# Performance work log

Hardware: AMD Instinct MI355X
Metric: run time of the kernel (lower is better)

The kernel has to match this reference:

```python
import jax, jax.numpy as jnp
import numpy as np
from math import sqrt

N_HEAD = 16
W_SCALE = 0.02  # keep pre-softmax logits in a sane range

def setup_inputs() -> dict:
    key = jax.random.key(0)
    ks = jax.random.split(key, 7)
    B, T, C = 2, 2048, 1024
    QL, KVL = 512, 512
    return {
        "x":     jax.random.normal(ks[0], (B, T, C), dtype=jnp.float32),
        "W_dq":  jax.random.normal(ks[1], (QL, C),  dtype=jnp.float32) * W_SCALE,
        "W_uq":  jax.random.normal(ks[2], (C, QL),  dtype=jnp.float32) * W_SCALE,
        "W_dkv": jax.random.normal(ks[3], (KVL, C), dtype=jnp.float32) * W_SCALE,
        "W_uk":  jax.random.normal(ks[4], (C, KVL), dtype=jnp.float32) * W_SCALE,
        "W_uv":  jax.random.normal(ks[5], (C, KVL), dtype=jnp.float32) * W_SCALE,
        "W_o":   jax.random.normal(ks[6], (C, C),   dtype=jnp.float32) * W_SCALE,
    }

def reference(x, W_dq, W_uq, W_dkv, W_uk, W_uv, W_o):
    B, T, C = x.shape
    nh = N_HEAD
    hs = C // nh
    n_kvl = W_dkv.shape[0]

    # absorbed matrices (training path of the torch module)
    # k_eff: (W_dq^T @ W_uq^T @ W_uk) -> (C, n_kvl) -> (nh, hs, n_kvl)
    k_eff = (W_dq.T @ W_uq.T @ W_uk).reshape(nh, hs, n_kvl)
    # v_eff: (W_uv^T @ W_o^T) -> (n_kvl, C) -> (n_kvl, nh, hs) -> (nh, n_kvl, hs)
    v_eff = jnp.transpose((W_uv.T @ W_o.T).reshape(n_kvl, nh, hs), (1, 0, 2))

    c_kv = x @ W_dkv.T                      # (B, T, n_kvl) latent KV cache
    q = (x @ W_dq.T) @ W_uq.T               # (B, T, C)
    q = q.reshape(B, T, nh, hs)             # (B, T, nh, hs)

    # scores: q @ k_eff @ c_kv^T / sqrt(hs) -> (B, nh, T, T)
    q_lat = jnp.einsum('bqhd,hdl->bhql', q, k_eff)
    attn = jnp.einsum('bhql,bkl->bhqk', q_lat, c_kv) / sqrt(hs)

    causal = jnp.tril(jnp.ones((T, T), dtype=bool))
    attn = jnp.where(causal[None, None], attn, -jnp.inf)
    attn = jax.nn.softmax(attn, axis=-1)    # dropout p=0.0

    # y = attn @ c_kv @ v_eff (W_o is absorbed into v_eff)
    y_lat = jnp.einsum('bhqk,bkl->bhql', attn, c_kv)
    y = jnp.einsum('bhql,hld->bqhd', y_lat, v_eff).reshape(B, T, C)
    return (y, c_kv)
```

## Files before the change

kernel.cpp:

```cpp
#include <hip/hip_runtime.h>
#include <hip/hip_bf16.h>


using bf16 = __hip_bfloat16;
using u32  = unsigned int;
using short8 = __attribute__((ext_vector_type(8))) short;
using f4     = __attribute__((ext_vector_type(4))) float;

static constexpr int kB  = 2;
static constexpr int kT  = 2048;
static constexpr int kC  = 1024;
static constexpr int kNH = 16;
static constexpr int kL  = 512;

__device__ inline u32 f2bf2(float a, float b) {
  bf16 ha = __float2bfloat16(a), hb = __float2bfloat16(b);
  unsigned short ua, ub;
  __builtin_memcpy(&ua, &ha, 2);
  __builtin_memcpy(&ub, &hb, 2);
  return (u32)ua | ((u32)ub << 16);
}
__device__ inline unsigned short f2bf(float x) {
  bf16 h = __float2bfloat16(x);
  unsigned short u; __builtin_memcpy(&u, &h, 2);
  return u;
}
__device__ inline short8 frag_ld(const void* p) {
  short8 r; __builtin_memcpy(&r, p, 16); return r;
}
__device__ inline void g2lds16(const bf16* g, bf16* l) {
  __builtin_amdgcn_global_load_lds(
      (const __attribute__((address_space(1))) u32*)g,
      (__attribute__((address_space(3))) u32*)l, 16, 0, 0);
}

__global__ __launch_bounds__(256)
void casts_merged(const float* __restrict__ x,   const float* __restrict__ wdq,
                  const float* __restrict__ wuq, const float* __restrict__ wdkv,
                  const float* __restrict__ wo,  const float* __restrict__ wuk,
                  const float* __restrict__ wuv,
                  bf16* __restrict__ xb,   bf16* __restrict__ wdqb,
                  bf16* __restrict__ wuqb, bf16* __restrict__ wdkvb,
                  bf16* __restrict__ wob,
                  bf16* __restrict__ uqT, bf16* __restrict__ ukT,
                  bf16* __restrict__ uvT, bf16* __restrict__ dqT)
{
  __shared__ float s[32][33];
  const int id = blockIdx.x;
  if (id < 6656) {
    long i = (long)(id * 256 + threadIdx.x) * 4;
    const float* sp; bf16* d; long off;
    if      (i < 4194304) { sp = x;    d = xb;    off = i; }
    else if (i < 4718592) { sp = wdq;  d = wdqb;  off = i - 4194304; }
    else if (i < 5242880) { sp = wuq;  d = wuqb;  off = i - 4718592; }
    else if (i < 5767168) { sp = wdkv; d = wdkvb; off = i - 5242880; }
    else                  { sp = wo;   d = wob;   off = i - 5767168; }
    float4 v = *(const float4*)(sp + off);
    *(uint2*)((u32*)d + off / 2) = make_uint2(f2bf2(v.x, v.y), f2bf2(v.z, v.w));
  } else {
    const int t = id - 6656;
    const int z = t >> 10, xy = t & 1023;
    const float* src = z == 0 ? wuq : z == 1 ? wuk : z == 2 ? wuv : wdq;
    bf16* dst        = z == 0 ? uqT : z == 1 ? ukT : z == 2 ? uvT : dqT;
    const int R = (z == 3) ? 512 : 1024, C = (z == 3) ? 1024 : 512;
    const int r0 = (xy & 31) * 32, c0 = (xy >> 5) * 32;
    if (r0 >= R || c0 >= C) return;
    const int xl = threadIdx.x & 31, y = threadIdx.x >> 5;
#pragma unroll
    for (int i = 0; i < 4; ++i)
      s[y*4 + i][xl] = src[(long)(r0 + y*4 + i) * C + c0 + xl];
    __syncthreads();
    unsigned short* dp = (unsigned short*)dst;
#pragma unroll
    for (int i = 0; i < 4; ++i)
      dp[(long)(c0 + y*4 + i) * R + r0 + xl] = f2bf(s[xl][y*4 + i]);
  }
}

__global__ __launch_bounds__(256)
void upcast_kernel(const bf16* __restrict__ qc, float* __restrict__ dst)
{
  int i = (blockIdx.x * 256 + threadIdx.x) * 4;
  if (i < 2097152) {
    int row = i >> 9, col = i & 511;
    uint2 v = *(const uint2*)((const u32*)(qc + (long)row * 1024 + 512 + col));
    float4 o;
    o.x = __uint_as_float(v.x << 16);
    o.y = __uint_as_float(v.x & 0xffff0000u);
    o.z = __uint_as_float(v.y << 16);
    o.w = __uint_as_float(v.y & 0xffff0000u);
    *(float4*)(dst + i) = o;
  }
}

template<typename TCe>
__global__ __launch_bounds__(256)
void mm_nt(const bf16* __restrict__ A, int lda, long aHi, long aLo,
           const bf16* __restrict__ Bm, int ldb, long bHi, long bLo,
           TCe* __restrict__ Cm, int ldc, long cHi, long cLo,
           int K, float alpha)
{
  const int z = blockIdx.z;
  A  += (long)(z >> 4) * aHi + (long)(z & 15) * aLo;
  Bm += (long)(z >> 4) * bHi + (long)(z & 15) * bLo;
  Cm += (long)(z >> 4) * cHi + (long)(z & 15) * cLo;

  __shared__ __align__(16) bf16 As[64][72];
  __shared__ __align__(16) bf16 Bs[64][72];

  const int tid = threadIdx.x;
  const int w = tid >> 6, lane = tid & 63;
  const int quad = lane >> 4, lp = lane & 15;
  const int m0 = blockIdx.x * 64, n0 = blockIdx.y * 64;
  const int row = tid >> 2, cseg = (tid & 3) * 16;

  f4 acc[4];
#pragma unroll
  for (int i = 0; i < 4; ++i) acc[i] = f4{0.f, 0.f, 0.f, 0.f};

  for (int k0 = 0; k0 < K; k0 += 64) {
    const bf16* ag = A  + (long)(m0 + row) * lda + k0 + cseg;
    const bf16* bg = Bm + (long)(n0 + row) * ldb + k0 + cseg;
    uint4 a0 = *(const uint4*)ag, a1 = *(const uint4*)(ag + 8);
    uint4 b0 = *(const uint4*)bg, b1 = *(const uint4*)(bg + 8);
    __syncthreads();
    *(uint4*)&As[row][cseg] = a0; *(uint4*)&As[row][cseg + 8] = a1;
    *(uint4*)&Bs[row][cseg] = b0; *(uint4*)&Bs[row][cseg + 8] = b1;
    __syncthreads();

    short8 af0 = frag_ld(&As[w*16 + lp][quad * 8]);
    short8 af1 = frag_ld(&As[w*16 + lp][32 + quad * 8]);
#pragma unroll
    for (int nb = 0; nb < 4; ++nb) {
      short8 bf0 = frag_ld(&Bs[nb*16 + lp][quad * 8]);
      short8 bf1 = frag_ld(&Bs[nb*16 + lp][32 + quad * 8]);
      acc[nb] = __builtin_amdgcn_mfma_f32_16x16x32_bf16(af0, bf0, acc[nb], 0, 0, 0);
      acc[nb] = __builtin_amdgcn_mfma_f32_16x16x32_bf16(af1, bf1, acc[nb], 0, 0, 0);
    }
  }
#pragma unroll
  for (int nb = 0; nb < 4; ++nb)
#pragma unroll
    for (int r = 0; r < 4; ++r) {
      float v = alpha * acc[nb][r];
      long off = (long)(m0 + w*16 + quad*4 + r) * ldc + n0 + nb*16 + lp;
      if constexpr (__is_same(TCe, float)) Cm[off] = v;
      else ((unsigned short*)Cm)[off] = f2bf(v);
    }
}

__global__ __launch_bounds__(256)
void mega1(const bf16* __restrict__ xb,   const bf16* __restrict__ wdq,
           const bf16* __restrict__ wukT, const bf16* __restrict__ wuqT,
           const bf16* __restrict__ wo,   const bf16* __restrict__ wuvT,
           bf16* __restrict__ qc, bf16* __restrict__ tmpT,
           bf16* __restrict__ v_effT)
{
  const int id = blockIdx.x;
  const bf16 *A, *Bm; bf16* Cm;
  int lda, ldb, ldc, m0, n0;
  if (id < 1024) {
    m0 = (id & 63) * 64; n0 = (id >> 6) * 64;
    A = xb;   lda = 1024; Bm = wdq;  ldb = 1024; Cm = qc;     ldc = 1024;
  } else if (id < 1088) {
    const int t = id - 1024;
    m0 = (t & 7) * 64; n0 = (t >> 3) * 64;
    A = wukT; lda = 1024; Bm = wuqT; ldb = 1024; Cm = tmpT;   ldc = 512;
  } else {
    const int t = id - 1088;
    m0 = (t & 15) * 64; n0 = (t >> 4) * 64;
    A = wo;   lda = 1024; Bm = wuvT; ldb = 1024; Cm = v_effT; ldc = 512;
  }

  __shared__ __align__(16) bf16 As[64][72];
  __shared__ __align__(16) bf16 Bs[64][72];

  const int tid = threadIdx.x;
  const int w = tid >> 6, lane = tid & 63;
  const int quad = lane >> 4, lp = lane & 15;
  const int row = tid >> 2, cseg = (tid & 3) * 16;

  f4 acc[4];
#pragma unroll
  for (int i = 0; i < 4; ++i) acc[i] = f4{0.f, 0.f, 0.f, 0.f};

  for (int k0 = 0; k0 < 1024; k0 += 64) {
    const bf16* ag = A  + (long)(m0 + row) * lda + k0 + cseg;
    const bf16* bg = Bm + (long)(n0 + row) * ldb + k0 + cseg;
    uint4 a0 = *(const uint4*)ag, a1 = *(const uint4*)(ag + 8);
    uint4 b0 = *(const uint4*)bg, b1 = *(const uint4*)(bg + 8);
    __syncthreads();
    *(uint4*)&As[row][cseg] = a0; *(uint4*)&As[row][cseg + 8] = a1;
    *(uint4*)&Bs[row][cseg] = b0; *(uint4*)&Bs[row][cseg + 8] = b1;
    __syncthreads();

    short8 af0 = frag_ld(&As[w*16 + lp][quad * 8]);
    short8 af1 = frag_ld(&As[w*16 + lp][32 + quad * 8]);
#pragma unroll
    for (int nb = 0; nb < 4; ++nb) {
      short8 bf0 = frag_ld(&Bs[nb*16 + lp][quad * 8]);
      short8 bf1 = frag_ld(&Bs[nb*16 + lp][32 + quad * 8]);
      acc[nb] = __builtin_amdgcn_mfma_f32_16x16x32_bf16(af0, bf0, acc[nb], 0, 0, 0);
      acc[nb] = __builtin_amdgcn_mfma_f32_16x16x32_bf16(af1, bf1, acc[nb], 0, 0, 0);
    }
  }
#pragma unroll
  for (int nb = 0; nb < 4; ++nb)
#pragma unroll
    for (int r = 0; r < 4; ++r) {
      long off = (long)(m0 + w*16 + quad*4 + r) * ldc + n0 + nb*16 + lp;
      ((unsigned short*)Cm)[off] = f2bf(acc[nb][r]);
    }
}

__global__ __launch_bounds__(256)
void gemm_multi(const bf16* __restrict__ qc,   const bf16* __restrict__ wuq,
                const bf16* __restrict__ keff, const bf16* __restrict__ veff,
                bf16* __restrict__ qfull, bf16* __restrict__ Kh,
                bf16* __restrict__ Vh, float kScale)
{
  const int id = blockIdx.x;
  const bf16 *A, *Bm; bf16* Cm;
  int lda, ldb, ldc, m0, n0; float alpha;
  if (id < 256) {
    m0 = (id >> 3) * 128; n0 = (id & 7) * 128;
    A = qc;        lda = 1024; Bm = wuq;  ldb = 512;
    Cm = qfull;    ldc = 1024; alpha = 1.0f;
  } else if (id < 512) {
    const int t = id - 256;
    m0 = (t >> 3) * 128; n0 = (t & 7) * 128;
    A = qc + 512;  lda = 1024; Bm = keff; ldb = 512;
    Cm = Kh;       ldc = 1024; alpha = kScale;
  } else {
    const int t = id - 512;
    const int b = t >> 7, tt = t & 127;
    m0 = (tt >> 4) * 128; n0 = (tt & 15) * 128;
    A = veff;      lda = 512;
    Bm = qc + (long)b * kT * 1024 + 512; ldb = 1024;
    Cm = Vh + (long)b * 1024 * kT;       ldc = kT; alpha = 1.0f;
  }

  __shared__ __align__(16) bf16 As[128 * 64];
  __shared__ __align__(16) bf16 Bs[128 * 64];

  const int tid = threadIdx.x;
  const int w = tid >> 6, lane = tid & 63;
  const int quad = lane >> 4, lp = lane & 15;
  const int wm = w >> 1, wn = w & 1;

  const int srow = lane >> 3;
  const int scol = ((lane & 7) ^ srow) * 8;
  const bf16* aSrc = A  + (long)(m0 + w * 32 + srow) * lda + scol;
  const bf16* bSrc = Bm + (long)(n0 + w * 32 + srow) * ldb + scol;
  bf16* aDst = As + w * 32 * 64;
  bf16* bDst = Bs + w * 32 * 64;

  f4 acc[4][4];
#pragma unroll
  for (int mi = 0; mi < 4; ++mi)
#pragma unroll
    for (int ni = 0; ni < 4; ++ni) acc[mi][ni] = f4{0.f, 0.f, 0.f, 0.f};

  const int swz = lp & 7;
  const int aRow = (wm * 64 + lp) * 64;
  const int bRow = (wn * 64 + lp) * 64;
  const int c0 = (quad       ^ swz) * 8;
  const int c1 = ((quad + 4) ^ swz) * 8;

  for (int k0 = 0; k0 < 512; k0 += 64) {
#pragma unroll
    for (int i = 0; i < 4; ++i) {
      g2lds16(aSrc + k0 + (long)(i * 8) * lda, aDst + i * 8 * 64);
      g2lds16(bSrc + k0 + (long)(i * 8) * ldb, bDst + i * 8 * 64);
    }
    asm volatile("s_waitcnt vmcnt(0)" ::: "memory");
    __builtin_amdgcn_s_barrier();

    short8 af0[4], af1[4], bf0[4], bf1[4];
#pragma unroll
    for (int mi = 0; mi < 4; ++mi) {
      af0[mi] = frag_ld(&As[aRow + mi * 1024 + c0]);
      af1[mi] = frag_ld(&As[aRow + mi * 1024 + c1]);
    }
#pragma unroll
    for (int ni = 0; ni < 4; ++ni) {
      bf0[ni] = frag_ld(&Bs[bRow + ni * 1024 + c0]);
      bf1[ni] = frag_ld(&Bs[bRow + ni * 1024 + c1]);
    }
#pragma unroll
    for (int mi = 0; mi < 4; ++mi)
#pragma unroll
      for (int ni = 0; ni < 4; ++ni) {
        acc[mi][ni] = __builtin_amdgcn_mfma_f32_16x16x32_bf16(
            af0[mi], bf0[ni], acc[mi][ni], 0, 0, 0);
        acc[mi][ni] = __builtin_amdgcn_mfma_f32_16x16x32_bf16(
            af1[mi], bf1[ni], acc[mi][ni], 0, 0, 0);
      }
    __builtin_amdgcn_s_barrier();
  }

#pragma unroll
  for (int mi = 0; mi < 4; ++mi)
#pragma unroll
    for (int ni = 0; ni < 4; ++ni)
#pragma unroll
      for (int r = 0; r < 4; ++r) {
        float v = alpha * acc[mi][ni][r];
        long off = (long)(m0 + wm*64 + mi*16 + quad*4 + r) * ldc
                 + n0 + wn*64 + ni*16 + lp;
        ((unsigned short*)Cm)[off] = f2bf(v);
      }
}

__global__ __launch_bounds__(512, 6)
void flash64(const bf16* __restrict__ qfull, const bf16* __restrict__ Kh,
             const bf16* __restrict__ VhT, float* __restrict__ y)
{
  const int id = blockIdx.x;
  const int j = id & 255, hi2 = id >> 8;
  const int h = j >> 4, sl = j & 15;
  const int s = hi2 ? (15 - sl) : sl;
  const int b = hi2;
  const int tid = threadIdx.x;
  const int w = tid >> 6, lane = tid & 63;
  const int quad = lane >> 4, lp = lane & 15;

  __shared__ __align__(16) bf16 Kt[2][64 * 64];
  __shared__ __align__(16) bf16 Vt[2][64 * 64];
  __shared__ __align__(16) bf16 Pb[8][16 * 72];

  bf16* Pw = &Pb[w][0];

  const long bh = (long)b * kNH + h;
  const int q0 = s * 128 + w * 16;

  const bf16* qp = qfull + ((long)b * kT + q0 + lp) * kC + h * 64 + quad * 8;
  const short8 qf0 = frag_ld(qp);
  const short8 qf1 = frag_ld(qp + 32);

  const int rk = w * 8 + (lane >> 3), blk = lane & 7;
  const int soff = ((blk ^ (rk & 7)) * 8);
  const bf16* kSrc = Kh + ((long)b * kT + rk) * kC + h * 64 + soff;
  const bf16* vSrc = VhT + (bh * 64 + rk) * (long)kT + soff;

  const int swz = lp & 7;
  const int lp64 = lp * 64;
  const int B0 = ((0 + quad) ^ swz) * 8;
  const int B1 = ((4 + quad) ^ swz) * 8;

  const int tmaxw = 2 * s + ((w >> 2) ? 1 : 0);
  const int nt = 2 * s + 2;

  f4 O0 = f4{0,0,0,0}, O1 = f4{0,0,0,0}, O2 = f4{0,0,0,0}, O3 = f4{0,0,0,0};
  float m_r = -3e38f, l_r = 0.f;

  g2lds16(kSrc, &Kt[0][w * 512]);
  g2lds16(vSrc, &Vt[0][w * 512]);
  asm volatile("s_waitcnt vmcnt(0)" ::: "memory");
  __builtin_amdgcn_s_barrier();
  __builtin_amdgcn_sched_barrier(0);

  for (int t = 0; t < nt; ++t) {
    const int bf = t & 1;
    if (t + 1 < nt) {
      g2lds16(kSrc + (long)(t + 1) * 65536, &Kt[bf ^ 1][w * 512]);
      g2lds16(vSrc + (t + 1) * 64,          &Vt[bf ^ 1][w * 512]);
    }

    if (t <= tmaxw) {
      const bf16* KB = &Kt[bf][0];
      f4 s0 = f4{0,0,0,0}, s1 = f4{0,0,0,0}, s2 = f4{0,0,0,0}, s3 = f4{0,0,0,0};
      {
        short8 a;
        a = frag_ld(KB +    0 + lp64 + B0); s0 = __builtin_amdgcn_mfma_f32_16x16x32_bf16(a, qf0, s0, 0, 0, 0);
        a = frag_ld(KB +    0 + lp64 + B1); s0 = __builtin_amdgcn_mfma_f32_16x16x32_bf16(a, qf1, s0, 0, 0, 0);
        a = frag_ld(KB + 1024 + lp64 + B0); s1 = __builtin_amdgcn_mfma_f32_16x16x32_bf16(a, qf0, s1, 0, 0, 0);
        a = frag_ld(KB + 1024 + lp64 + B1); s1 = __builtin_amdgcn_mfma_f32_16x16x32_bf16(a, qf1, s1, 0, 0, 0);
        a = frag_ld(KB + 2048 + lp64 + B0); s2 = __builtin_amdgcn_mfma_f32_16x16x32_bf16(a, qf0, s2, 0, 0, 0);
        a = frag_ld(KB + 2048 + lp64 + B1); s2 = __builtin_amdgcn_mfma_f32_16x16x32_bf16(a, qf1, s2, 0, 0, 0);
        a = frag_ld(KB + 3072 + lp64 + B0); s3 = __builtin_amdgcn_mfma_f32_16x16x32_bf16(a, qf0, s3, 0, 0, 0);
        a = frag_ld(KB + 3072 + lp64 + B1); s3 = __builtin_amdgcn_mfma_f32_16x16x32_bf16(a, qf1, s3, 0, 0, 0);
      }

      if (t == tmaxw) {
        const int kb = t * 64, q = q0 + lp;
#pragma unroll
        for (int r = 0; r < 4; ++r) {
          if (kb +      quad * 4 + r > q) s0[r] = -3e38f;
          if (kb + 16 + quad * 4 + r > q) s1[r] = -3e38f;
          if (kb + 32 + quad * 4 + r > q) s2[r] = -3e38f;
          if (kb + 48 + quad * 4 + r > q) s3[r] = -3e38f;
        }
      }

      float tm = fmaxf(fmaxf(fmaxf(s0[0], s0[1]), fmaxf(s0[2], s0[3])),
                       fmaxf(fmaxf(s1[0], s1[1]), fmaxf(s1[2], s1[3])));
      tm = fmaxf(tm, fmaxf(fmaxf(fmaxf(s2[0], s2[1]), fmaxf(s2[2], s2[3])),
                           fmaxf(fmaxf(s3[0], s3[1]), fmaxf(s3[2], s3[3]))));
      tm = fmaxf(tm, __shfl_xor(tm, 16, 64));
      tm = fmaxf(tm, __shfl_xor(tm, 32, 64));
      if (__ballot(tm > m_r + 12.0f)) {
        float mn = fmaxf(m_r, tm);
        float al = exp2f(m_r - mn);
        l_r *= al; m_r = mn;
#pragma unroll
        for (int jj = 0; jj < 4; ++jj) {
          O0[jj] *= al; O1[jj] *= al; O2[jj] *= al; O3[jj] *= al;
        }
      }
      float p0[4], p1[4], p2[4], p3[4], rs = 0.f;
#pragma unroll
      for (int r = 0; r < 4; ++r) {
        p0[r] = exp2f(s0[r] - m_r); p1[r] = exp2f(s1[r] - m_r);
        p2[r] = exp2f(s2[r] - m_r); p3[r] = exp2f(s3[r] - m_r);
        rs += p0[r] + p1[r] + p2[r] + p3[r];
      }
      rs += __shfl_xor(rs, 16, 64);
      rs += __shfl_xor(rs, 32, 64);
      l_r += rs;

      {
        bf16* pr = Pw + lp * 72 + quad * 4;
        *(uint2*)(pr)      = make_uint2(f2bf2(p0[0], p0[1]), f2bf2(p0[2], p0[3]));
        *(uint2*)(pr + 16) = make_uint2(f2bf2(p1[0], p1[1]), f2bf2(p1[2], p1[3]));
        *(uint2*)(pr + 32) = make_uint2(f2bf2(p2[0], p2[1]), f2bf2(p2[2], p2[3]));
        *(uint2*)(pr + 48) = make_uint2(f2bf2(p3[0], p3[1]), f2bf2(p3[2], p3[3]));
      }
      asm volatile("s_waitcnt lgkmcnt(0)" ::: "memory");
      short8 pb0 = frag_ld(Pw + lp * 72 + quad * 8);
      short8 pb1 = frag_ld(Pw + lp * 72 + 32 + quad * 8);

      const bf16* VB = &Vt[bf][0];
      {
        short8 a;
        a = frag_ld(VB +    0 + lp64 + B0); O0 = __builtin_amdgcn_mfma_f32_16x16x32_bf16(a, pb0, O0, 0, 0, 0);
        a = frag_ld(VB +    0 + lp64 + B1); O0 = __builtin_amdgcn_mfma_f32_16x16x32_bf16(a, pb1, O0, 0, 0, 0);
        a = frag_ld(VB + 1024 + lp64 + B0); O1 = __builtin_amdgcn_mfma_f32_16x16x32_bf16(a, pb0, O1, 0, 0, 0);
        a = frag_ld(VB + 1024 + lp64 + B1); O1 = __builtin_amdgcn_mfma_f32_16x16x32_bf16(a, pb1, O1, 0, 0, 0);
        a = frag_ld(VB + 2048 + lp64 + B0); O2 = __builtin_amdgcn_mfma_f32_16x16x32_bf16(a, pb0, O2, 0, 0, 0);
        a = frag_ld(VB + 2048 + lp64 + B1); O2 = __builtin_amdgcn_mfma_f32_16x16x32_bf16(a, pb1, O2, 0, 0, 0);
        a = frag_ld(VB + 3072 + lp64 + B0); O3 = __builtin_amdgcn_mfma_f32_16x16x32_bf16(a, pb0, O3, 0, 0, 0);
        a = frag_ld(VB + 3072 + lp64 + B1); O3 = __builtin_amdgcn_mfma_f32_16x16x32_bf16(a, pb1, O3, 0, 0, 0);
      }
    }

    asm volatile("s_waitcnt vmcnt(0)" ::: "memory");
    __builtin_amdgcn_s_barrier();
    __builtin_amdgcn_sched_barrier(0);
  }

  {
    const float inv = 1.0f / l_r;
    float* yp = y + ((long)b * kT + q0 + lp) * kC + h * 64 + quad * 4;
    *(float4*)(yp +  0) = float4{O0[0]*inv, O0[1]*inv, O0[2]*inv, O0[3]*inv};
    *(float4*)(yp + 16) = float4{O1[0]*inv, O1[1]*inv, O1[2]*inv, O1[3]*inv};
    *(float4*)(yp + 32) = float4{O2[0]*inv, O2[1]*inv, O2[2]*inv, O2[3]*inv};
    *(float4*)(yp + 48) = float4{O3[0]*inv, O3[1]*inv, O3[2]*inv, O3[3]*inv};
  }
}

extern "C" void kernel_launch(void* const* d_in, const int* in_sizes, int n_in,
                              void* d_out, int out_size, void* d_ws, size_t ws_size,
                              hipStream_t stream)
{
  const float* x     = (const float*)d_in[0];
  const float* W_dq  = (const float*)d_in[1];
  const float* W_uq  = (const float*)d_in[2];
  const float* W_dkv = (const float*)d_in[3];
  const float* W_uk  = (const float*)d_in[4];
  const float* W_uv  = (const float*)d_in[5];
  const float* W_o   = (const float*)d_in[6];

  float* y_out   = (float*)d_out;
  float* ckv_out = y_out + (long)kB * kT * kC;

  char* ws = (char*)d_ws;
  bf16* qc      = (bf16*)(ws + 0);
  bf16* qfullb  = (bf16*)(ws + 8388608);
  bf16* K_head  = (bf16*)(ws + 16777216);
  bf16* V_headT = (bf16*)(ws + 25165824);
  bf16* xb      = (bf16*)(ws + 33554432);
  bf16* W_dqb   = (bf16*)(ws + 41943040);
  bf16* W_dkvb  = (bf16*)(ws + 42991616);
  bf16* W_uqb   = (bf16*)(ws + 44040192);
  bf16* W_ob    = (bf16*)(ws + 45088768);
  bf16* W_uqTb  = (bf16*)(ws + 47185920);
  bf16* W_ukTb  = (bf16*)(ws + 48234496);
  bf16* W_uvTb  = (bf16*)(ws + 49283072);
  bf16* W_dqTb  = (bf16*)(ws + 50331648);
  bf16* tmpT    = (bf16*)(ws + 51380224);
  bf16* k_effF  = (bf16*)(ws + 51904512);
  bf16* v_effT  = (bf16*)(ws + 52953088);

  const dim3 blk(256);
  const float kScale = 0.125f * 1.44269504088896f;

  casts_merged<<<dim3(10752), blk, 0, stream>>>(
      x, W_dq, W_uq, W_dkv, W_o, W_uk, W_uv,
      xb, W_dqb, W_uqb, W_dkvb, W_ob,
      W_uqTb, W_ukTb, W_uvTb, W_dqTb);

  mega1<<<dim3(1216), blk, 0, stream>>>(
      xb, W_dqb, W_ukTb, W_uqTb, W_ob, W_uvTb, qc, tmpT, v_effT);

  mm_nt<bf16><<<dim3(16, 8, 1), blk, 0, stream>>>(
      W_dqTb, 512, 0, 0, tmpT, 512, 0, 0, k_effF, 512, 0, 0, 512, 1.0f);

  gemm_multi<<<dim3(768), blk, 0, stream>>>(
      qc, W_uqb, k_effF, v_effT, qfullb, K_head, V_headT, kScale);

  flash64<<<dim3(512), dim3(512), 0, stream>>>(
      qfullb, K_head, V_headT, y_out);

  upcast_kernel<<<dim3(2048), blk, 0, stream>>>(qc, ckv_out);

  (void)in_sizes; (void)n_in; (void)out_size; (void)ws_size;
}
```

Baseline: 201.8 us.

## Shrink flash blocks to 64 queries and fuse c_kv fp32 output into GEMM

The flash-attention kernel now uses 256-thread blocks, each covering 64 query rows, with 1024 blocks ordered largest-causal-work first. Each wave loads twice as many K/V rows into LDS per tile, and the per-wave tile skip logic is no longer needed. This aims at better load balance and occupancy across CUs. Separately, the fp32 c_kv output is written straight from the mega1 GEMM epilogue, which removes the upcast kernel launch and its re-read of qc; the cost is extra scattered fp32 stores in that epilogue.

```diff
diff --git a/kernel.cpp b/kernel.cpp
--- a/kernel.cpp
+++ b/kernel.cpp
@@ -77,22 +77,6 @@
   }
 }
 
-__global__ __launch_bounds__(256)
-void upcast_kernel(const bf16* __restrict__ qc, float* __restrict__ dst)
-{
-  int i = (blockIdx.x * 256 + threadIdx.x) * 4;
-  if (i < 2097152) {
-    int row = i >> 9, col = i & 511;
-    uint2 v = *(const uint2*)((const u32*)(qc + (long)row * 1024 + 512 + col));
-    float4 o;
-    o.x = __uint_as_float(v.x << 16);
-    o.y = __uint_as_float(v.x & 0xffff0000u);
-    o.z = __uint_as_float(v.y << 16);
-    o.w = __uint_as_float(v.y & 0xffff0000u);
-    *(float4*)(dst + i) = o;
-  }
-}
-
 template<typename TCe>
 __global__ __launch_bounds__(256)
 void mm_nt(const bf16* __restrict__ A, int lda, long aHi, long aLo,
@@ -154,14 +138,16 @@
            const bf16* __restrict__ wukT, const bf16* __restrict__ wuqT,
            const bf16* __restrict__ wo,   const bf16* __restrict__ wuvT,
            bf16* __restrict__ qc, bf16* __restrict__ tmpT,
-           bf16* __restrict__ v_effT)
+           bf16* __restrict__ v_effT, float* __restrict__ ckv_out)
 {
   const int id = blockIdx.x;
   const bf16 *A, *Bm; bf16* Cm;
   int lda, ldb, ldc, m0, n0;
+  bool wckv = false;
   if (id < 1024) {
     m0 = (id & 63) * 64; n0 = (id >> 6) * 64;
     A = xb;   lda = 1024; Bm = wdq;  ldb = 1024; Cm = qc;     ldc = 1024;
+    wckv = (n0 >= 512);
   } else if (id < 1088) {
     const int t = id - 1024;
     m0 = (t & 7) * 64; n0 = (t >> 3) * 64;
@@ -208,8 +194,12 @@
   for (int nb = 0; nb < 4; ++nb)
 #pragma unroll
     for (int r = 0; r < 4; ++r) {
-      long off = (long)(m0 + w*16 + quad*4 + r) * ldc + n0 + nb*16 + lp;
-      ((unsigned short*)Cm)[off] = f2bf(acc[nb][r]);
+      float v = acc[nb][r];
+      const int rr = m0 + w*16 + quad*4 + r;
+      long off = (long)rr * ldc + n0 + nb*16 + lp;
+      ((unsigned short*)Cm)[off] = f2bf(v);
+      if (wckv)
+        ckv_out[(long)rr * 512 + (n0 - 512) + nb*16 + lp] = v;
     }
 }
 
@@ -312,50 +302,50 @@
       }
 }
 
-__global__ __launch_bounds__(512, 6)
+__global__ __launch_bounds__(256, 3)
 void flash64(const bf16* __restrict__ qfull, const bf16* __restrict__ Kh,
              const bf16* __restrict__ VhT, float* __restrict__ y)
 {
   const int id = blockIdx.x;
-  const int j = id & 255, hi2 = id >> 8;
-  const int h = j >> 4, sl = j & 15;
-  const int s = hi2 ? (15 - sl) : sl;
-  const int b = hi2;
+  const int qblk = 31 - (id >> 5);
+  const int bh = id & 31;
+  const int b = bh >> 4, h = bh & 15;
   const int tid = threadIdx.x;
   const int w = tid >> 6, lane = tid & 63;
   const int quad = lane >> 4, lp = lane & 15;
 
   __shared__ __align__(16) bf16 Kt[2][64 * 64];
   __shared__ __align__(16) bf16 Vt[2][64 * 64];
-  __shared__ __align__(16) bf16 Pb[8][16 * 72];
+  __shared__ __align__(16) bf16 Pb[4][16 * 72];
 
   bf16* Pw = &Pb[w][0];
 
-  const long bh = (long)b * kNH + h;
-  const int q0 = s * 128 + w * 16;
+  const long bhl = (long)b * kNH + h;
+  const int q0 = qblk * 64 + w * 16;
 
   const bf16* qp = qfull + ((long)b * kT + q0 + lp) * kC + h * 64 + quad * 8;
   const short8 qf0 = frag_ld(qp);
   const short8 qf1 = frag_ld(qp + 32);
 
-  const int rk = w * 8 + (lane >> 3), blk = lane & 7;
+  const int rk = w * 16 + (lane >> 3), blk = lane & 7;
   const int soff = ((blk ^ (rk & 7)) * 8);
   const bf16* kSrc = Kh + ((long)b * kT + rk) * kC + h * 64 + soff;
-  const bf16* vSrc = VhT + (bh * 64 + rk) * (long)kT + soff;
+  const bf16* vSrc = VhT + (bhl * 64 + rk) * (long)kT + soff;
 
   const int swz = lp & 7;
   const int lp64 = lp * 64;
   const int B0 = ((0 + quad) ^ swz) * 8;
   const int B1 = ((4 + quad) ^ swz) * 8;
 
-  const int tmaxw = 2 * s + ((w >> 2) ? 1 : 0);
-  const int nt = 2 * s + 2;
+  const int nt = qblk + 1;
 
   f4 O0 = f4{0,0,0,0}, O1 = f4{0,0,0,0}, O2 = f4{0,0,0,0}, O3 = f4{0,0,0,0};
   float m_r = -3e38f, l_r = 0.f;
 
-  g2lds16(kSrc, &Kt[0][w * 512]);
-  g2lds16(vSrc, &Vt[0][w * 512]);
+  g2lds16(kSrc,            &Kt[0][w * 1024]);
+  g2lds16(kSrc + 8 * kC,   &Kt[0][w * 1024 + 512]);
+  g2lds16(vSrc,            &Vt[0][w * 1024]);
+  g2lds16(vSrc + 8 * kT,   &Vt[0][w * 1024 + 512]);
   asm volatile("s_waitcnt vmcnt(0)" ::: "memory");
   __builtin_amdgcn_s_barrier();
   __builtin_amdgcn_sched_barrier(0);
@@ -363,11 +353,15 @@
   for (int t = 0; t < nt; ++t) {
     const int bf = t & 1;
     if (t + 1 < nt) {
-      g2lds16(kSrc + (long)(t + 1) * 65536, &Kt[bf ^ 1][w * 512]);
-      g2lds16(vSrc + (t + 1) * 64,          &Vt[bf ^ 1][w * 512]);
-    }
-
-    if (t <= tmaxw) {
+      const bf16* k1 = kSrc + (long)(t + 1) * 65536;
+      const bf16* v1 = vSrc + (t + 1) * 64;
+      g2lds16(k1,          &Kt[bf ^ 1][w * 1024]);
+      g2lds16(k1 + 8 * kC, &Kt[bf ^ 1][w * 1024 + 512]);
+      g2lds16(v1,          &Vt[bf ^ 1][w * 1024]);
+      g2lds16(v1 + 8 * kT, &Vt[bf ^ 1][w * 1024 + 512]);
+    }
+
+    {
       const bf16* KB = &Kt[bf][0];
       f4 s0 = f4{0,0,0,0}, s1 = f4{0,0,0,0}, s2 = f4{0,0,0,0}, s3 = f4{0,0,0,0};
       {
@@ -382,7 +376,7 @@
         a = frag_ld(KB + 3072 + lp64 + B1); s3 = __builtin_amdgcn_mfma_f32_16x16x32_bf16(a, qf1, s3, 0, 0, 0);
       }
 
-      if (t == tmaxw) {
+      if (t == qblk) {
         const int kb = t * 64, q = q0 + lp;
 #pragma unroll
         for (int r = 0; r < 4; ++r) {
@@ -501,7 +495,7 @@
       W_uqTb, W_ukTb, W_uvTb, W_dqTb);
 
   mega1<<<dim3(1216), blk, 0, stream>>>(
-      xb, W_dqb, W_ukTb, W_uqTb, W_ob, W_uvTb, qc, tmpT, v_effT);
+      xb, W_dqb, W_ukTb, W_uqTb, W_ob, W_uvTb, qc, tmpT, v_effT, ckv_out);
 
   mm_nt<bf16><<<dim3(16, 8, 1), blk, 0, stream>>>(
       W_dqTb, 512, 0, 0, tmpT, 512, 0, 0, k_effF, 512, 0, 0, 512, 1.0f);
@@ -509,10 +503,8 @@
   gemm_multi<<<dim3(768), blk, 0, stream>>>(
       qc, W_uqb, k_effF, v_effT, qfullb, K_head, V_headT, kScale);
 
-  flash64<<<dim3(512), dim3(512), 0, stream>>>(
+  flash64<<<dim3(1024), dim3(256), 0, stream>>>(
       qfullb, K_head, V_headT, y_out);
 
-  upcast_kernel<<<dim3(2048), blk, 0, stream>>>(qc, ckv_out);
-
   (void)in_sizes; (void)n_in; (void)out_size; (void)ws_size;
 }
```

Measured after the change: 187.0 us. -7.3%, faster.
